# Optimization experiments

Measured on AMD Instinct MI355X. Metric: run time of the kernel, lower is better.

## Reference

```python
import jax, jax.numpy as jnp
import numpy as np

B, N, M, DN, DE, WN, WE, P = 16, 128, 1024, 512, 256, 128, 128, 512
EMB = WN + WE            # nenn embedding size per node / per edge
CLS_IN = 2 * EMB // 1    # = 2*wn + 2*we = 512
LR_OUT, CR_OUT, MR_OUT = 9, 6, 17
HID = 256


def _mk_params(key):
    ks = jax.random.split(key, 16)
    s = 0.02
    p = {
        'Wn':  jax.random.normal(ks[0], (DN, WN), jnp.float32) * s,
        'We':  jax.random.normal(ks[1], (DE, WE), jnp.float32) * s,
        'Wn2': jax.random.normal(ks[2], (DN, WN), jnp.float32) * s,
        'We2': jax.random.normal(ks[3], (DE, WE), jnp.float32) * s,
    }
    for i, h in enumerate(['scr', 'lr', 'mr']):
        out = {'scr': CR_OUT, 'lr': LR_OUT, 'mr': MR_OUT}[h]
        p[h + '_W1'] = jax.random.normal(ks[4 + 4 * i], (2 * EMB, HID), jnp.float32) * s
        p[h + '_b1'] = jnp.zeros((HID,), jnp.float32)
        p[h + '_W2'] = jax.random.normal(ks[5 + 4 * i], (HID, out), jnp.float32) * s
        p[h + '_b2'] = jnp.zeros((out,), jnp.float32)
    return p


def setup_inputs() -> dict:
    key = jax.random.key(0)
    ks = jax.random.split(key, 10)
    inp = {
        'node_features': jax.random.normal(ks[0], (B, N, DN), jnp.float32),
        'edge_features': jax.random.normal(ks[1], (B, N, N, DE), jnp.float32),
        'adj_mat': (jax.random.uniform(ks[2], (B, N, N)) < 0.1).astype(jnp.float32),
        'line_adj_mat': (jax.random.uniform(ks[3], (B, M, M)) < 0.02).astype(jnp.float32),
        'edge_index': jax.random.randint(ks[4], (B, 2, M), 0, N, jnp.int32),
        'object_pairs': jax.random.randint(ks[5], (B, P, 2), 0, N, jnp.int32),
        'num_obj': jax.random.randint(ks[6], (B,), N // 4, N + 1, jnp.int32),
        'num_edges': jax.random.randint(ks[7], (B,), M // 4, M + 1, jnp.int32),
    }
    inp.update(_mk_params(ks[8]))
    return inp


def _mlp(x, W1, b1, W2, b2):
    return jax.nn.relu(x @ W1 + b1) @ W2 + b2


def _forward(node_features, edge_features, adj_mat, line_adj_mat,
             Wn, We, Wn2, We2,
             scr_W1, scr_b1, scr_W2, scr_b2,
             lr_W1, lr_b1, lr_W2, lr_b2,
             mr_W1, mr_b1, mr_W2, mr_b2,
             edge_index, object_pairs, num_obj, num_edges):
    dt = node_features.dtype
    # ragged slicing [:num_obj] / [:num_edges] expressed as masks (padding stays 0)
    nmask = (jnp.arange(N) < num_obj[:, None]).astype(dt)      # [B,N]
    emask = (jnp.arange(M) < num_edges[:, None]).astype(dt)    # [B,M]

    X = node_features * nmask[..., None]                        # [B,N,DN]
    A = (adj_mat * nmask[:, :, None] * nmask[:, None, :]
         + jnp.eye(N, dtype=dt)[None] * nmask[:, :, None])      # A + I, masked
    h = jax.nn.relu((A @ X) @ Wn) * nmask[..., None]            # [B,N,WN] node-level emb

    src, dst = edge_index[:, 0], edge_index[:, 1]               # [B,M]
    Eg = jax.vmap(lambda e, s, d: e[s, d])(edge_features, src, dst)  # [B,M,DE]
    Eg = Eg * emask[..., None]
    L = (line_adj_mat * emask[:, :, None] * emask[:, None, :]
         + jnp.eye(M, dtype=dt)[None] * emask[:, :, None])      # line graph A + I
    g = jax.nn.relu((L @ Eg) @ We) * emask[..., None]           # [B,M,WE] edge-level emb

    # aggregate edge embeddings onto their source nodes (ragged scatter-add)
    agg = jax.vmap(lambda gb, sb: jnp.zeros((N, WE), gb.dtype).at[sb].add(gb))(g, src)
    node_emb = jnp.concatenate([h, agg * nmask[..., None]], -1)  # [B,N,EMB]

    # dense pairwise edge embeddings [B,N,N,EMB]
    Xp = X @ Wn2                                                 # [B,N,WN]
    Pm = jax.nn.relu(Xp[:, :, None, :] + Xp[:, None, :, :])      # node part [B,N,N,WN]
    Q = jax.nn.relu(edge_features @ We2)                         # edge part [B,N,N,WE]
    edge_emb = jnp.concatenate([Pm, Q], -1)

    # make_classifier_inputs: fused ragged gather instead of python double loop
    p0, p1 = object_pairs[..., 0], object_pairs[..., 1]          # [B,P]
    emb0 = jnp.take_along_axis(node_emb, p0[:, :, None], axis=1)  # [B,P,EMB]
    emb1 = jnp.take_along_axis(node_emb, p1[:, :, None], axis=1)
    eedge = jax.vmap(lambda eb, a, b: eb[a, b])(edge_emb, p0, p1)  # [B,P,EMB]
    ci = jnp.concatenate([emb0 + emb1, eedge], -1)               # aggregator='sum'

    lr = _mlp(ci, lr_W1, lr_b1, lr_W2, lr_b2)
    cr = _mlp(ci, scr_W1, scr_b1, scr_W2, scr_b2)
    mr = _mlp(ci, mr_W1, mr_b1, mr_W2, mr_b2)
    return lr, cr, mr


def reference(node_features, edge_features, adj_mat, line_adj_mat,
              edge_index, object_pairs, num_obj, num_edges,
              Wn, We, Wn2, We2,
              scr_W1, scr_b1, scr_W2, scr_b2,
              lr_W1, lr_b1, lr_W2, lr_b2,
              mr_W1, mr_b1, mr_W2, mr_b2):
    return _forward(node_features, edge_features, adj_mat, line_adj_mat,
                    Wn, We, Wn2, We2,
                    scr_W1, scr_b1, scr_W2, scr_b2,
                    lr_W1, lr_b1, lr_W2, lr_b2,
                    mr_W1, mr_b1, mr_W2, mr_b2,
                    edge_index, object_pairs, num_obj, num_edges)
```

## Files before the change

### kernel.cpp

```cpp
#include <hip/hip_runtime.h>
#include <hip/hip_bf16.h>
#include <cstdint>
#include <cstddef>

#define BB 16
#define NN 128
#define MM 1024
#define DN 512
#define DE 256
#define WN 128
#define WE 128
#define PP 512
#define HIDW 256
#define CIW 512

typedef __attribute__((ext_vector_type(8))) short s16x8;
typedef __attribute__((ext_vector_type(4))) float f32x4;

__device__ __forceinline__ float bf2f(unsigned short u) {
    unsigned int x = ((unsigned int)u) << 16;
    union { unsigned int i; float f; } c; c.i = x; return c.f;
}
__device__ __forceinline__ short f2b(float f) {
    __hip_bfloat16 h = __float2bfloat16(f);
    return *reinterpret_cast<short*>(&h);
}

__device__ __forceinline__ void gl_lds16(const ushort* g, ushort* l) {
    __builtin_amdgcn_global_load_lds(
        (const __attribute__((address_space(1))) unsigned int*)g,
        (__attribute__((address_space(3))) unsigned int*)l,
        16, 0, 0);
}

__global__ __launch_bounds__(256) void k0_prep(
    const float* __restrict__ lrW1, const float* __restrict__ scrW1,
    const float* __restrict__ mrW1,
    const float* __restrict__ lrb1, const float* __restrict__ scrb1,
    const float* __restrict__ mrb1,
    const float* __restrict__ Wn, const float* __restrict__ Wn2,
    const float* __restrict__ We, const float* __restrict__ We2,
    __hip_bfloat16* __restrict__ W1t, __hip_bfloat16* __restrict__ WncT,
    __hip_bfloat16* __restrict__ WeT, __hip_bfloat16* __restrict__ We2T,
    float* __restrict__ b1cat)
{
    int blk = blockIdx.x;
    int t = threadIdx.x;
    if (blk < 768) {
        int h = blk >> 8, n = blk & 255;
        const float* W = (h == 0) ? lrW1 : (h == 1) ? scrW1 : mrW1;
        W1t[(size_t)blk * 512 + t]       = __float2bfloat16(W[t * 256 + n]);
        W1t[(size_t)blk * 512 + t + 256] = __float2bfloat16(W[(t + 256) * 256 + n]);
    } else if (blk == 768) {
        b1cat[t]       = lrb1[t];
        b1cat[256 + t] = scrb1[t];
        b1cat[512 + t] = mrb1[t];
    } else if (blk < 897) {
        int n = blk - 769;
        WeT[(size_t)n * 256 + t] = __float2bfloat16(We[t * 128 + n]);
    } else if (blk < 1153) {
        int n = blk - 897;
        const float* W = (n < 128) ? Wn : Wn2;
        int c = n & 127;
        WncT[(size_t)n * 512 + t]       = __float2bfloat16(W[t * 128 + c]);
        WncT[(size_t)n * 512 + t + 256] = __float2bfloat16(W[(t + 256) * 128 + c]);
    } else {
        int n = blk - 1153;
        We2T[(size_t)n * 256 + t] = __float2bfloat16(We2[t * 128 + n]);
    }
}

__global__ __launch_bounds__(256) void fproj(
    const float* __restrict__ nf, const float* __restrict__ ef,
    const int* __restrict__ eidx, const int* __restrict__ opair,
    const int* __restrict__ nobj, const int* __restrict__ nedg,
    const ushort* __restrict__ WncT, const ushort* __restrict__ WeT,
    const ushort* __restrict__ We2T,
    float* __restrict__ Y, float* __restrict__ Xp,
    float* __restrict__ G1, __hip_bfloat16* __restrict__ ci)
{
    __shared__ ushort As[128 * 32];
    __shared__ ushort Bs[128 * 32];
    __shared__ unsigned rowoff[128];
    __shared__ float    rowval[128];

    int blk = blockIdx.x;
    int route, mb, nb, K;
    const ushort* Bt;
    if (blk < 32)       { route = 0; mb = blk >> 1;  nb = blk & 1; K = 512; Bt = WncT; }
    else if (blk < 160) { route = 1; mb = blk - 32;  nb = 0;       K = 256; Bt = WeT;  }
    else                { route = 2; mb = blk - 160; nb = 0;       K = 256; Bt = We2T; }
    int row0 = mb * 128, col0 = nb * 128;
    int t = threadIdx.x;

    if (t < 128) {
        int r = row0 + t;
        unsigned off; float valid = 1.f;
        if (route == 0) {
            int b = r >> 7, i = r & 127;
            off = (unsigned)r * DN;
            valid = (i < nobj[b]) ? 1.f : 0.f;
        } else if (route == 1) {
            int b = r >> 10, m = r & 1023;
            int src = eidx[b * 2 * MM + m];
            int dst = eidx[b * 2 * MM + MM + m];
            off = (unsigned)((b * NN + src) * NN + dst) * DE;
            valid = (m < nedg[b]) ? 1.f : 0.f;
        } else {
            int r2 = r;
            int b = r2 >> 9, p = r2 & 511;
            int i0 = opair[(b * PP + p) * 2];
            int i1 = opair[(b * PP + p) * 2 + 1];
            off = (unsigned)((b * NN + i0) * NN + i1) * DE;
        }
        rowoff[t] = off; rowval[t] = valid;
    }

    const float* Asrc = (route == 0) ? nf : ef;
    int lane = t & 63;
    int w    = t >> 6;
    int wr   = w >> 1, wc = w & 1;
    int arow = w * 32 + (lane >> 2);
    int ak   = (lane & 3) * 8;
    int qk   = (lane >> 4) * 8;
    int fr   = lane & 15;
    int sr   = t >> 2;
    int sk   = (t & 3) * 8;
    f32x4 acc[4][4];
    #pragma unroll
    for (int i = 0; i < 4; ++i)
        #pragma unroll
        for (int j = 0; j < 4; ++j) acc[i][j] = (f32x4){0.f, 0.f, 0.f, 0.f};

    for (int k0 = 0; k0 < K; k0 += 32) {
        __syncthreads();
        gl_lds16(&Bt[(size_t)(col0 + sr) * K + k0 + sk],      &Bs[t * 8]);
        gl_lds16(&Bt[(size_t)(col0 + sr + 64) * K + k0 + sk], &Bs[t * 8 + 2048]);
        {
            unsigned o0 = rowoff[arow] + k0 + ak;
            unsigned o1 = rowoff[arow + 16] + k0 + ak;
            float m0 = rowval[arow], m1 = rowval[arow + 16];
            float4 a0 = *(const float4*)&Asrc[o0];
            float4 a1 = *(const float4*)&Asrc[o0 + 4];
            float4 b0 = *(const float4*)&Asrc[o1];
            float4 b1 = *(const float4*)&Asrc[o1 + 4];
            s16x8 pa, pb;
            pa[0]=f2b(a0.x*m0); pa[1]=f2b(a0.y*m0); pa[2]=f2b(a0.z*m0); pa[3]=f2b(a0.w*m0);
            pa[4]=f2b(a1.x*m0); pa[5]=f2b(a1.y*m0); pa[6]=f2b(a1.z*m0); pa[7]=f2b(a1.w*m0);
            pb[0]=f2b(b0.x*m1); pb[1]=f2b(b0.y*m1); pb[2]=f2b(b0.z*m1); pb[3]=f2b(b0.w*m1);
            pb[4]=f2b(b1.x*m1); pb[5]=f2b(b1.y*m1); pb[6]=f2b(b1.z*m1); pb[7]=f2b(b1.w*m1);
            *(s16x8*)&As[arow * 32 + ak]        = pa;
            *(s16x8*)&As[(arow + 16) * 32 + ak] = pb;
        }
        __syncthreads();
        s16x8 af[4], bfv[4];
        #pragma unroll
        for (int mi = 0; mi < 4; ++mi)
            af[mi] = *(const s16x8*)&As[(wr * 64 + mi * 16 + fr) * 32 + qk];
        #pragma unroll
        for (int ni = 0; ni < 4; ++ni)
            bfv[ni] = *(const s16x8*)&Bs[(wc * 64 + ni * 16 + fr) * 32 + qk];
        #pragma unroll
        for (int mi = 0; mi < 4; ++mi)
            #pragma unroll
            for (int ni = 0; ni < 4; ++ni)
                acc[mi][ni] = __builtin_amdgcn_mfma_f32_16x16x32_bf16(
                    af[mi], bfv[ni], acc[mi][ni], 0, 0, 0);
    }
    int crow = (lane >> 4) * 4;
    #pragma unroll
    for (int mi = 0; mi < 4; ++mi) {
        #pragma unroll
        for (int ni = 0; ni < 4; ++ni) {
            int gc = col0 + wc * 64 + ni * 16 + fr;
            int gr = row0 + wr * 64 + mi * 16 + crow;
            #pragma unroll
            for (int rg = 0; rg < 4; ++rg) {
                float v = acc[mi][ni][rg];
                int r = gr + rg;
                if (route == 0) {
                    if (gc < 128) Y [(size_t)r * WN + gc]       = v;
                    else          Xp[(size_t)r * WN + gc - 128] = v;
                } else if (route == 1) {
                    G1[(size_t)r * WE + gc] = v;
                } else {
                    ci[(size_t)r * CIW + 384 + gc] = __float2bfloat16(fmaxf(v, 0.f));
                }
            }
        }
    }
}

__global__ __launch_bounds__(256) void k2_gcn_node(
    const float* __restrict__ adj, const int* __restrict__ num_obj,
    const float* __restrict__ Y, float* __restrict__ node_emb)
{
    __shared__ float As[16 * 129];
    int b  = blockIdx.x >> 4;
    int i0 = ((blockIdx.x >> 1) & 7) * 16;
    int ch = blockIdx.x & 1;
    int s  = num_obj[b];
    int t  = threadIdx.x;
    if (t < 128) {
        for (int rr = 0; rr < 16; ++rr) {
            int i = i0 + rr;
            float v = 0.f;
            if (i < s) {
                v = adj[(size_t)(b * NN + i) * NN + t] * ((t < s) ? 1.f : 0.f);
                if (t == i) v += 1.f;
            }
            As[rr * 129 + t] = v;
        }
    }
    __syncthreads();
    int c  = ch * 64 + (t & 63);
    int rb = (t >> 6) * 4;
    float acc[4] = {0.f,0.f,0.f,0.f};
    for (int j = 0; j < NN; ++j) {
        float yv = Y[(b * NN + j) * WN + c];
        #pragma unroll
        for (int r = 0; r < 4; ++r) acc[r] += As[(rb + r) * 129 + j] * yv;
    }
    #pragma unroll
    for (int r = 0; r < 4; ++r) {
        int i = i0 + rb + r;
        node_emb[(b * NN + i) * 256 + c]       = fmaxf(acc[r], 0.f);
        node_emb[(b * NN + i) * 256 + 128 + c] = 0.f;
    }
}

__global__ __launch_bounds__(128) void k4_line_gcn(
    const float* __restrict__ la, const float* __restrict__ G1,
    const int* __restrict__ eidx, const int* __restrict__ num_edges,
    float* __restrict__ node_emb)
{
    int b = blockIdx.x >> 10;
    int m = blockIdx.x & 1023;
    int se = num_edges[b];
    if (m >= se) return;
    __shared__ int   cnt;
    __shared__ int   idxs[MM];
    __shared__ float vals[MM];
    int t = threadIdx.x;
    if (t == 0) cnt = 0;
    __syncthreads();
    const float* larow = la + ((size_t)b * MM + m) * MM;
    for (int it = 0; it < 8; ++it) {
        int j = it * 128 + t;
        float v = larow[j];
        if (v != 0.f) {
            int pos = atomicAdd(&cnt, 1);
            idxs[pos] = j;
            vals[pos] = v;
        }
    }
    __syncthreads();
    int n = cnt;
    const float* g1b = G1 + (size_t)b * MM * WE;
    float acc = g1b[m * WE + t];
    for (int p = 0; p < n; ++p)
        acc += vals[p] * g1b[idxs[p] * WE + t];
    float g = fmaxf(acc, 0.f);
    int src = eidx[b * 2 * MM + m];
    atomicAdd(&node_emb[(b * NN + src) * 256 + 128 + t], g);
}

__global__ __launch_bounds__(256) void k5a_build_ci(
    const float* __restrict__ node_emb, const float* __restrict__ Xp,
    const int* __restrict__ opairs, const int* __restrict__ num_obj,
    __hip_bfloat16* __restrict__ ci)
{
    __shared__ int   pi0[16], pi1[16];
    __shared__ float nm0[16], nm1[16];
    int b     = blockIdx.x >> 5;
    int pbase = (blockIdx.x & 31) * 16;
    int t     = threadIdx.x;
    int s     = num_obj[b];
    if (t < 16) {
        int p  = pbase + t;
        int i0 = opairs[(b * PP + p) * 2];
        int i1 = opairs[(b * PP + p) * 2 + 1];
        pi0[t] = i0; pi1[t] = i1;
        nm0[t] = (i0 < s) ? 1.f : 0.f;
        nm1[t] = (i1 < s) ? 1.f : 0.f;
    }
    __syncthreads();
    for (int pp = 0; pp < 16; ++pp) {
        int i0 = pi0[pp], i1 = pi1[pp];
        int p  = pbase + pp;
        __hip_bfloat16* cirow = ci + (size_t)(b * PP + p) * CIW;
        float m0f = (t < 128) ? 1.f : nm0[pp];
        float m1f = (t < 128) ? 1.f : nm1[pp];
        float v = node_emb[(b * NN + i0) * 256 + t] * m0f
                + node_emb[(b * NN + i1) * 256 + t] * m1f;
        cirow[t] = __float2bfloat16(v);
        if (t < 128) {
            float pm = Xp[(b * NN + i0) * WN + t] + Xp[(b * NN + i1) * WN + t];
            cirow[256 + t] = __float2bfloat16(fmaxf(pm, 0.f));
        }
    }
}

__global__ __launch_bounds__(256) void k6_mlp1_mfma(
    const ushort* __restrict__ A,
    const ushort* __restrict__ Bt,
    const float* __restrict__ b1cat,
    __hip_bfloat16* __restrict__ H)
{
    __shared__ ushort As[128 * 32];
    __shared__ ushort Bs[128 * 32];
    int t    = threadIdx.x;
    int col0 = blockIdx.x * 128;
    int row0 = blockIdx.y * 128;
    int lane = t & 63;
    int w    = t >> 6;
    int wr   = w >> 1, wc = w & 1;
    int qk   = (lane >> 4) * 8;
    int fr   = lane & 15;
    int sr   = t >> 2;
    int sk   = (t & 3) * 8;
    f32x4 acc[4][4];
    #pragma unroll
    for (int i = 0; i < 4; ++i)
        #pragma unroll
        for (int j = 0; j < 4; ++j) acc[i][j] = (f32x4){0.f, 0.f, 0.f, 0.f};

    for (int k0 = 0; k0 < CIW; k0 += 32) {
        __syncthreads();
        gl_lds16(&A [(size_t)(row0 + sr) * CIW + k0 + sk],      &As[t * 8]);
        gl_lds16(&A [(size_t)(row0 + sr + 64) * CIW + k0 + sk], &As[t * 8 + 2048]);
        gl_lds16(&Bt[(size_t)(col0 + sr) * CIW + k0 + sk],      &Bs[t * 8]);
        gl_lds16(&Bt[(size_t)(col0 + sr + 64) * CIW + k0 + sk], &Bs[t * 8 + 2048]);
        __syncthreads();
        s16x8 af[4], bfv[4];
        #pragma unroll
        for (int mi = 0; mi < 4; ++mi)
            af[mi] = *(const s16x8*)&As[(wr * 64 + mi * 16 + fr) * 32 + qk];
        #pragma unroll
        for (int ni = 0; ni < 4; ++ni)
            bfv[ni] = *(const s16x8*)&Bs[(wc * 64 + ni * 16 + fr) * 32 + qk];
        #pragma unroll
        for (int mi = 0; mi < 4; ++mi)
            #pragma unroll
            for (int ni = 0; ni < 4; ++ni)
                acc[mi][ni] = __builtin_amdgcn_mfma_f32_16x16x32_bf16(
                    af[mi], bfv[ni], acc[mi][ni], 0, 0, 0);
    }
    int crow = (lane >> 4) * 4;
    #pragma unroll
    for (int mi = 0; mi < 4; ++mi) {
        #pragma unroll
        for (int ni = 0; ni < 4; ++ni) {
            int gc = col0 + wc * 64 + ni * 16 + fr;
            int gr = row0 + wr * 64 + mi * 16 + crow;
            float bias = b1cat[gc];
            #pragma unroll
            for (int rg = 0; rg < 4; ++rg) {
                float v = fmaxf(acc[mi][ni][rg] + bias, 0.f);
                H[(size_t)(gr + rg) * 768 + gc] = __float2bfloat16(v);
            }
        }
    }
}

__global__ __launch_bounds__(256) void k7_mlp2(
    const __hip_bfloat16* __restrict__ H,
    const float* __restrict__ lrW2, const float* __restrict__ lrb2,
    const float* __restrict__ scrW2, const float* __restrict__ scrb2,
    const float* __restrict__ mrW2, const float* __restrict__ mrb2,
    float* __restrict__ outp)
{
    __shared__ float w2s[32 * 257];
    int t = threadIdx.x;
    for (int o = 0; o < 32; ++o) {
        float v;
        if (o < 9)       v = lrW2[t * 9 + o];
        else if (o < 15) v = scrW2[t * 6 + (o - 9)];
        else             v = mrW2[t * 17 + (o - 15)];
        w2s[o * 257 + t] = v;
    }
    __syncthreads();
    int p = blockIdx.x * 8 + (t >> 5);
    int o = t & 31;
    int seg = (o < 9) ? 0 : ((o < 15) ? 1 : 2);
    const ushort* hr = (const ushort*)H + (size_t)p * 768 + seg * 256;
    const float* wr = &w2s[o * 257];
    float acc = (o < 9) ? lrb2[o] : ((o < 15) ? scrb2[o - 9] : mrb2[o - 15]);
    for (int k = 0; k < HIDW; k += 8) {
        s16x8 u = *(const s16x8*)&hr[k];
        acc += bf2f((unsigned short)u[0]) * wr[k]
             + bf2f((unsigned short)u[1]) * wr[k + 1]
             + bf2f((unsigned short)u[2]) * wr[k + 2]
             + bf2f((unsigned short)u[3]) * wr[k + 3]
             + bf2f((unsigned short)u[4]) * wr[k + 4]
             + bf2f((unsigned short)u[5]) * wr[k + 5]
             + bf2f((unsigned short)u[6]) * wr[k + 6]
             + bf2f((unsigned short)u[7]) * wr[k + 7];
    }
    if (o < 9)       outp[(size_t)p * 9 + o] = acc;
    else if (o < 15) outp[8192 * 9 + (size_t)p * 6 + (o - 9)] = acc;
    else             outp[8192 * 15 + (size_t)p * 17 + (o - 15)] = acc;
}

extern "C" void kernel_launch(void* const* d_in, const int* in_sizes, int n_in,
                              void* d_out, int out_size, void* d_ws, size_t ws_size,
                              hipStream_t stream) {
    const float* nf    = (const float*)d_in[0];
    const float* ef    = (const float*)d_in[1];
    const float* adj   = (const float*)d_in[2];
    const float* la    = (const float*)d_in[3];
    const int*   eidx  = (const int*)d_in[4];
    const int*   opair = (const int*)d_in[5];
    const int*   nobj  = (const int*)d_in[6];
    const int*   nedg  = (const int*)d_in[7];
    const float* Wn    = (const float*)d_in[8];
    const float* We    = (const float*)d_in[9];
    const float* Wn2   = (const float*)d_in[10];
    const float* We2   = (const float*)d_in[11];
    const float* scrW1 = (const float*)d_in[12];
    const float* scrb1 = (const float*)d_in[13];
    const float* scrW2 = (const float*)d_in[14];
    const float* scrb2 = (const float*)d_in[15];
    const float* lrW1  = (const float*)d_in[16];
    const float* lrb1  = (const float*)d_in[17];
    const float* lrW2  = (const float*)d_in[18];
    const float* lrb2  = (const float*)d_in[19];
    const float* mrW1  = (const float*)d_in[20];
    const float* mrb1  = (const float*)d_in[21];
    const float* mrW2  = (const float*)d_in[22];
    const float* mrb2  = (const float*)d_in[23];

    float* ws = (float*)d_ws;
    float* Y        = ws;
    float* Xp       = Y + 262144;
    float* node_emb = Xp + 262144;
    float* G1       = node_emb + 524288;
    float* base     = G1 + 2097152;
    __hip_bfloat16* ci   = (__hip_bfloat16*)base;
    __hip_bfloat16* hid  = (__hip_bfloat16*)(base + 2097152);
    __hip_bfloat16* W1t  = (__hip_bfloat16*)(base + 2097152 + 3145728);
    __hip_bfloat16* WncT = (__hip_bfloat16*)(base + 2097152 + 3145728 + 196608);
    __hip_bfloat16* WeT  = (__hip_bfloat16*)(base + 2097152 + 3145728 + 196608 + 65536);
    __hip_bfloat16* We2T = (__hip_bfloat16*)(base + 2097152 + 3145728 + 196608 + 65536 + 16384);
    float* b1cat = base + 2097152 + 3145728 + 196608 + 65536 + 16384 + 16384;

    k0_prep <<<1281, 256, 0, stream>>>(lrW1, scrW1, mrW1, lrb1, scrb1, mrb1,
                                       Wn, Wn2, We, We2,
                                       W1t, WncT, WeT, We2T, b1cat);
    fproj   <<<224, 256, 0, stream>>>(nf, ef, eidx, opair, nobj, nedg,
                                      (const ushort*)WncT, (const ushort*)WeT,
                                      (const ushort*)We2T, Y, Xp, G1, ci);
    k2_gcn_node <<<BB * 8 * 2, 256, 0, stream>>>(adj, nobj, Y, node_emb);
    k4_line_gcn <<<BB * MM, 128, 0, stream>>>(la, G1, eidx, nedg, node_emb);
    k5a_build_ci<<<BB * (PP / 16), 256, 0, stream>>>(node_emb, Xp, opair, nobj, ci);
    k6_mlp1_mfma<<<dim3(6, 64), 256, 0, stream>>>((const ushort*)ci,
                                                  (const ushort*)W1t, b1cat, hid);
    k7_mlp2     <<<8192 / 8, 256, 0, stream>>>(hid, lrW2, lrb2, scrW2, scrb2,
                                               mrW2, mrb2, (float*)d_out);
}
```

Baseline: 473.1 us.

## Fuse all stages into one persistent kernel with software grid barriers

Replaces the seven separate kernel launches with a single persistent kernel of 384 blocks. Each former kernel becomes a phase that loops over its virtual blocks, and phases are separated by an atomic-counter grid barrier that is reset by a memset before launch. This is meant to remove launch overhead and the gaps between dependent kernels. In exchange, each phase is limited to 384 resident blocks, the kernel needs more LDS because it uses a union of all phase buffers, and correctness relies on every block being co-resident; the spin loop has a bounded timeout that silently breaks out.

```diff
diff --git a/kernel.cpp b/kernel.cpp
--- a/kernel.cpp
+++ b/kernel.cpp
@@ -14,6 +14,8 @@
 #define HIDW 256
 #define CIW 512
 
+#define NBLK 384
+
 typedef __attribute__((ext_vector_type(8))) short s16x8;
 typedef __attribute__((ext_vector_type(4))) float f32x4;
 
@@ -25,7 +27,6 @@
     __hip_bfloat16 h = __float2bfloat16(f);
     return *reinterpret_cast<short*>(&h);
 }
-
 __device__ __forceinline__ void gl_lds16(const ushort* g, ushort* l) {
     __builtin_amdgcn_global_load_lds(
         (const __attribute__((address_space(1))) unsigned int*)g,
@@ -33,403 +34,383 @@
         16, 0, 0);
 }
 
-__global__ __launch_bounds__(256) void k0_prep(
-    const float* __restrict__ lrW1, const float* __restrict__ scrW1,
-    const float* __restrict__ mrW1,
-    const float* __restrict__ lrb1, const float* __restrict__ scrb1,
-    const float* __restrict__ mrb1,
-    const float* __restrict__ Wn, const float* __restrict__ Wn2,
-    const float* __restrict__ We, const float* __restrict__ We2,
-    __hip_bfloat16* __restrict__ W1t, __hip_bfloat16* __restrict__ WncT,
-    __hip_bfloat16* __restrict__ WeT, __hip_bfloat16* __restrict__ We2T,
-    float* __restrict__ b1cat)
-{
-    int blk = blockIdx.x;
-    int t = threadIdx.x;
-    if (blk < 768) {
-        int h = blk >> 8, n = blk & 255;
-        const float* W = (h == 0) ? lrW1 : (h == 1) ? scrW1 : mrW1;
-        W1t[(size_t)blk * 512 + t]       = __float2bfloat16(W[t * 256 + n]);
-        W1t[(size_t)blk * 512 + t + 256] = __float2bfloat16(W[(t + 256) * 256 + n]);
-    } else if (blk == 768) {
-        b1cat[t]       = lrb1[t];
-        b1cat[256 + t] = scrb1[t];
-        b1cat[512 + t] = mrb1[t];
-    } else if (blk < 897) {
-        int n = blk - 769;
-        WeT[(size_t)n * 256 + t] = __float2bfloat16(We[t * 128 + n]);
-    } else if (blk < 1153) {
-        int n = blk - 897;
-        const float* W = (n < 128) ? Wn : Wn2;
-        int c = n & 127;
-        WncT[(size_t)n * 512 + t]       = __float2bfloat16(W[t * 128 + c]);
-        WncT[(size_t)n * 512 + t + 256] = __float2bfloat16(W[(t + 256) * 128 + c]);
-    } else {
-        int n = blk - 1153;
-        We2T[(size_t)n * 256 + t] = __float2bfloat16(We2[t * 128 + n]);
-    }
-}
-
-__global__ __launch_bounds__(256) void fproj(
-    const float* __restrict__ nf, const float* __restrict__ ef,
-    const int* __restrict__ eidx, const int* __restrict__ opair,
-    const int* __restrict__ nobj, const int* __restrict__ nedg,
-    const ushort* __restrict__ WncT, const ushort* __restrict__ WeT,
-    const ushort* __restrict__ We2T,
-    float* __restrict__ Y, float* __restrict__ Xp,
-    float* __restrict__ G1, __hip_bfloat16* __restrict__ ci)
-{
-    __shared__ ushort As[128 * 32];
-    __shared__ ushort Bs[128 * 32];
-    __shared__ unsigned rowoff[128];
-    __shared__ float    rowval[128];
-
-    int blk = blockIdx.x;
-    int route, mb, nb, K;
-    const ushort* Bt;
-    if (blk < 32)       { route = 0; mb = blk >> 1;  nb = blk & 1; K = 512; Bt = WncT; }
-    else if (blk < 160) { route = 1; mb = blk - 32;  nb = 0;       K = 256; Bt = WeT;  }
-    else                { route = 2; mb = blk - 160; nb = 0;       K = 256; Bt = We2T; }
-    int row0 = mb * 128, col0 = nb * 128;
-    int t = threadIdx.x;
-
-    if (t < 128) {
-        int r = row0 + t;
-        unsigned off; float valid = 1.f;
-        if (route == 0) {
-            int b = r >> 7, i = r & 127;
-            off = (unsigned)r * DN;
-            valid = (i < nobj[b]) ? 1.f : 0.f;
-        } else if (route == 1) {
-            int b = r >> 10, m = r & 1023;
-            int src = eidx[b * 2 * MM + m];
-            int dst = eidx[b * 2 * MM + MM + m];
-            off = (unsigned)((b * NN + src) * NN + dst) * DE;
-            valid = (m < nedg[b]) ? 1.f : 0.f;
+__device__ __forceinline__ void grid_barrier(unsigned* cnt, unsigned phase) {
+    __syncthreads();
+    if (threadIdx.x == 0) {
+        __threadfence();
+        __hip_atomic_fetch_add(cnt, 1u, __ATOMIC_ACQ_REL, __HIP_MEMORY_SCOPE_AGENT);
+        unsigned target = (unsigned)NBLK * (phase + 1u);
+        long spin = 0;
+        while (__hip_atomic_load(cnt, __ATOMIC_ACQUIRE, __HIP_MEMORY_SCOPE_AGENT) < target) {
+            __builtin_amdgcn_s_sleep(8);
+            if (++spin > (1L << 20)) break;
+        }
+        __threadfence();
+    }
+    __syncthreads();
+}
+
+struct MegaP {
+    const float *nf, *ef, *adj, *la;
+    const int *eidx, *opair, *nobj, *nedg;
+    const float *Wn, *We, *Wn2, *We2;
+    const float *scrW1, *scrb1, *scrW2, *scrb2;
+    const float *lrW1, *lrb1, *lrW2, *lrb2;
+    const float *mrW1, *mrb1, *mrW2, *mrb2;
+    float *Y, *Xp, *node_emb, *G1;
+    __hip_bfloat16 *ci, *hid, *W1t, *WncT, *WeT, *We2T;
+    float *b1cat;
+    unsigned *gbar;
+    float *outp;
+};
+
+union Smem {
+    struct { ushort As[128 * 32]; ushort Bs[128 * 32];
+             unsigned rowoff[128]; float rowval[128]; } g;
+    struct { float As[16 * 129]; } k2;
+    struct { int idxs[2][MM]; float vals[2][MM]; int cnt[2]; } k4;
+    struct { int pi0[16], pi1[16]; float nm0[16], nm1[16]; } k5;
+    struct { float w2s[32 * 257]; } k7;
+};
+
+__global__ __launch_bounds__(256, 2) void mega(MegaP P) {
+    __shared__ Smem S;
+    const int t   = threadIdx.x;
+    const int bid = blockIdx.x;
+    const int nb  = gridDim.x;
+
+    for (int vb = bid; vb < 1281; vb += nb) {
+        if (vb < 768) {
+            int h = vb >> 8, n = vb & 255;
+            const float* W = (h == 0) ? P.lrW1 : (h == 1) ? P.scrW1 : P.mrW1;
+            P.W1t[(size_t)vb * 512 + t]       = __float2bfloat16(W[t * 256 + n]);
+            P.W1t[(size_t)vb * 512 + t + 256] = __float2bfloat16(W[(t + 256) * 256 + n]);
+        } else if (vb == 768) {
+            P.b1cat[t]       = P.lrb1[t];
+            P.b1cat[256 + t] = P.scrb1[t];
+            P.b1cat[512 + t] = P.mrb1[t];
+        } else if (vb < 897) {
+            int n = vb - 769;
+            P.WeT[(size_t)n * 256 + t] = __float2bfloat16(P.We[t * 128 + n]);
+        } else if (vb < 1153) {
+            int n = vb - 897;
+            const float* W = (n < 128) ? P.Wn : P.Wn2;
+            int c = n & 127;
+            P.WncT[(size_t)n * 512 + t]       = __float2bfloat16(W[t * 128 + c]);
+            P.WncT[(size_t)n * 512 + t + 256] = __float2bfloat16(W[(t + 256) * 128 + c]);
         } else {
-            int r2 = r;
-            int b = r2 >> 9, p = r2 & 511;
-            int i0 = opair[(b * PP + p) * 2];
-            int i1 = opair[(b * PP + p) * 2 + 1];
-            off = (unsigned)((b * NN + i0) * NN + i1) * DE;
-        }
-        rowoff[t] = off; rowval[t] = valid;
-    }
-
-    const float* Asrc = (route == 0) ? nf : ef;
-    int lane = t & 63;
-    int w    = t >> 6;
-    int wr   = w >> 1, wc = w & 1;
-    int arow = w * 32 + (lane >> 2);
-    int ak   = (lane & 3) * 8;
-    int qk   = (lane >> 4) * 8;
-    int fr   = lane & 15;
-    int sr   = t >> 2;
-    int sk   = (t & 3) * 8;
-    f32x4 acc[4][4];
-    #pragma unroll
-    for (int i = 0; i < 4; ++i)
+            int n = vb - 1153;
+            P.We2T[(size_t)n * 256 + t] = __float2bfloat16(P.We2[t * 128 + n]);
+        }
+    }
+    grid_barrier(P.gbar, 0);
+
+    {
+        const int lane = t & 63, w = t >> 6;
+        const int wr = w >> 1, wc = w & 1;
+        const int arow = w * 32 + (lane >> 2);
+        const int ak = (lane & 3) * 8;
+        const int qk = (lane >> 4) * 8;
+        const int fr = lane & 15;
+        const int sr = t >> 2;
+        const int sk = (t & 3) * 8;
+        for (int vb = bid; vb < 224; vb += nb) {
+            int route, mb, nbk, K;
+            const ushort* Bt;
+            if (vb < 32)       { route = 0; mb = vb >> 1;  nbk = vb & 1; K = 512; Bt = (const ushort*)P.WncT; }
+            else if (vb < 160) { route = 1; mb = vb - 32;  nbk = 0;      K = 256; Bt = (const ushort*)P.WeT;  }
+            else               { route = 2; mb = vb - 160; nbk = 0;      K = 256; Bt = (const ushort*)P.We2T; }
+            int row0 = mb * 128, col0 = nbk * 128;
+            __syncthreads();
+            if (t < 128) {
+                int r = row0 + t;
+                unsigned off; float valid = 1.f;
+                if (route == 0) {
+                    int b = r >> 7, i = r & 127;
+                    off = (unsigned)r * DN;
+                    valid = (i < P.nobj[b]) ? 1.f : 0.f;
+                } else if (route == 1) {
+                    int b = r >> 10, m = r & 1023;
+                    int src = P.eidx[b * 2 * MM + m];
+                    int dst = P.eidx[b * 2 * MM + MM + m];
+                    off = (unsigned)((b * NN + src) * NN + dst) * DE;
+                    valid = (m < P.nedg[b]) ? 1.f : 0.f;
+                } else {
+                    int b = r >> 9, p = r & 511;
+                    int i0 = P.opair[(b * PP + p) * 2];
+                    int i1 = P.opair[(b * PP + p) * 2 + 1];
+                    off = (unsigned)((b * NN + i0) * NN + i1) * DE;
+                }
+                S.g.rowoff[t] = off; S.g.rowval[t] = valid;
+            }
+            const float* Asrc = (route == 0) ? P.nf : P.ef;
+            f32x4 acc[4][4];
+            #pragma unroll
+            for (int i = 0; i < 4; ++i)
+                #pragma unroll
+                for (int j = 0; j < 4; ++j) acc[i][j] = (f32x4){0.f, 0.f, 0.f, 0.f};
+
+            for (int k0 = 0; k0 < K; k0 += 32) {
+                __syncthreads();
+                gl_lds16(&Bt[(size_t)(col0 + sr) * K + k0 + sk],      &S.g.Bs[t * 8]);
+                gl_lds16(&Bt[(size_t)(col0 + sr + 64) * K + k0 + sk], &S.g.Bs[t * 8 + 2048]);
+                {
+                    unsigned o0 = S.g.rowoff[arow] + k0 + ak;
+                    unsigned o1 = S.g.rowoff[arow + 16] + k0 + ak;
+                    float m0 = S.g.rowval[arow], m1 = S.g.rowval[arow + 16];
+                    float4 a0 = *(const float4*)&Asrc[o0];
+                    float4 a1 = *(const float4*)&Asrc[o0 + 4];
+                    float4 b0 = *(const float4*)&Asrc[o1];
+                    float4 b1 = *(const float4*)&Asrc[o1 + 4];
+                    s16x8 pa, pb;
+                    pa[0]=f2b(a0.x*m0); pa[1]=f2b(a0.y*m0); pa[2]=f2b(a0.z*m0); pa[3]=f2b(a0.w*m0);
+                    pa[4]=f2b(a1.x*m0); pa[5]=f2b(a1.y*m0); pa[6]=f2b(a1.z*m0); pa[7]=f2b(a1.w*m0);
+                    pb[0]=f2b(b0.x*m1); pb[1]=f2b(b0.y*m1); pb[2]=f2b(b0.z*m1); pb[3]=f2b(b0.w*m1);
+                    pb[4]=f2b(b1.x*m1); pb[5]=f2b(b1.y*m1); pb[6]=f2b(b1.z*m1); pb[7]=f2b(b1.w*m1);
+                    *(s16x8*)&S.g.As[arow * 32 + ak]        = pa;
+                    *(s16x8*)&S.g.As[(arow + 16) * 32 + ak] = pb;
+                }
+                __syncthreads();
+                s16x8 af[4], bfv[4];
+                #pragma unroll
+                for (int mi = 0; mi < 4; ++mi)
+                    af[mi] = *(const s16x8*)&S.g.As[(wr * 64 + mi * 16 + fr) * 32 + qk];
+                #pragma unroll
+                for (int ni = 0; ni < 4; ++ni)
+                    bfv[ni] = *(const s16x8*)&S.g.Bs[(wc * 64 + ni * 16 + fr) * 32 + qk];
+                #pragma unroll
+                for (int mi = 0; mi < 4; ++mi)
+                    #pragma unroll
+                    for (int ni = 0; ni < 4; ++ni)
+                        acc[mi][ni] = __builtin_amdgcn_mfma_f32_16x16x32_bf16(
+                            af[mi], bfv[ni], acc[mi][ni], 0, 0, 0);
+            }
+            int crow = (lane >> 4) * 4;
+            #pragma unroll
+            for (int mi = 0; mi < 4; ++mi) {
+                #pragma unroll
+                for (int ni = 0; ni < 4; ++ni) {
+                    int gc = col0 + wc * 64 + ni * 16 + fr;
+                    int gr = row0 + wr * 64 + mi * 16 + crow;
+                    #pragma unroll
+                    for (int rg = 0; rg < 4; ++rg) {
+                        float v = acc[mi][ni][rg];
+                        int r = gr + rg;
+                        if (route == 0) {
+                            if (gc < 128) P.Y [(size_t)r * WN + gc]       = v;
+                            else          P.Xp[(size_t)r * WN + gc - 128] = v;
+                        } else if (route == 1) {
+                            P.G1[(size_t)r * WE + gc] = v;
+                        } else {
+                            P.ci[(size_t)r * CIW + 384 + gc] = __float2bfloat16(fmaxf(v, 0.f));
+                        }
+                    }
+                }
+            }
+        }
+    }
+    grid_barrier(P.gbar, 1);
+
+    for (int vb = bid; vb < 256; vb += nb) {
+        int b  = vb >> 4;
+        int i0 = ((vb >> 1) & 7) * 16;
+        int ch = vb & 1;
+        int s  = P.nobj[b];
+        __syncthreads();
+        if (t < 128) {
+            for (int rr = 0; rr < 16; ++rr) {
+                int i = i0 + rr;
+                float v = 0.f;
+                if (i < s) {
+                    v = P.adj[(size_t)(b * NN + i) * NN + t] * ((t < s) ? 1.f : 0.f);
+                    if (t == i) v += 1.f;
+                }
+                S.k2.As[rr * 129 + t] = v;
+            }
+        }
+        __syncthreads();
+        int c  = ch * 64 + (t & 63);
+        int rb = (t >> 6) * 4;
+        float acc[4] = {0.f, 0.f, 0.f, 0.f};
+        for (int j = 0; j < NN; ++j) {
+            float yv = P.Y[(b * NN + j) * WN + c];
+            #pragma unroll
+            for (int r = 0; r < 4; ++r) acc[r] += S.k2.As[(rb + r) * 129 + j] * yv;
+        }
         #pragma unroll
-        for (int j = 0; j < 4; ++j) acc[i][j] = (f32x4){0.f, 0.f, 0.f, 0.f};
-
-    for (int k0 = 0; k0 < K; k0 += 32) {
+        for (int r = 0; r < 4; ++r) {
+            int i = i0 + rb + r;
+            P.node_emb[(b * NN + i) * 256 + c]       = fmaxf(acc[r], 0.f);
+            P.node_emb[(b * NN + i) * 256 + 128 + c] = 0.f;
+        }
+    }
+    grid_barrier(P.gbar, 2);
+
+    {
+        const int half = t >> 7;
+        const int ch   = t & 127;
+        for (int vb = bid; vb < 8192; vb += nb) {
+            int b = vb >> 9;
+            int m = (vb & 511) * 2 + half;
+            int se = P.nedg[b];
+            bool act = (m < se);
+            __syncthreads();
+            if (ch == 0) S.k4.cnt[half] = 0;
+            __syncthreads();
+            if (act) {
+                const float4* larow = (const float4*)(P.la + ((size_t)b * MM + m) * MM);
+                #pragma unroll
+                for (int pass = 0; pass < 2; ++pass) {
+                    int j4 = pass * 128 + ch;
+                    float4 v = larow[j4];
+                    int j0 = j4 * 4;
+                    if (v.x != 0.f) { int p = atomicAdd(&S.k4.cnt[half], 1); S.k4.idxs[half][p] = j0;     S.k4.vals[half][p] = v.x; }
+                    if (v.y != 0.f) { int p = atomicAdd(&S.k4.cnt[half], 1); S.k4.idxs[half][p] = j0 + 1; S.k4.vals[half][p] = v.y; }
+                    if (v.z != 0.f) { int p = atomicAdd(&S.k4.cnt[half], 1); S.k4.idxs[half][p] = j0 + 2; S.k4.vals[half][p] = v.z; }
+                    if (v.w != 0.f) { int p = atomicAdd(&S.k4.cnt[half], 1); S.k4.idxs[half][p] = j0 + 3; S.k4.vals[half][p] = v.w; }
+                }
+            }
+            __syncthreads();
+            if (act) {
+                int n = S.k4.cnt[half];
+                const float* g1b = P.G1 + (size_t)b * MM * WE;
+                float acc = g1b[m * WE + ch];
+                for (int p = 0; p < n; ++p)
+                    acc += S.k4.vals[half][p] * g1b[S.k4.idxs[half][p] * WE + ch];
+                float gv = fmaxf(acc, 0.f);
+                int src = P.eidx[b * 2 * MM + m];
+                atomicAdd(&P.node_emb[((size_t)b * NN + src) * 256 + 128 + ch], gv);
+            }
+        }
+    }
+    grid_barrier(P.gbar, 3);
+
+    for (int vb = bid; vb < 512; vb += nb) {
+        int b     = vb >> 5;
+        int pbase = (vb & 31) * 16;
+        int s     = P.nobj[b];
         __syncthreads();
-        gl_lds16(&Bt[(size_t)(col0 + sr) * K + k0 + sk],      &Bs[t * 8]);
-        gl_lds16(&Bt[(size_t)(col0 + sr + 64) * K + k0 + sk], &Bs[t * 8 + 2048]);
-        {
-            unsigned o0 = rowoff[arow] + k0 + ak;
-            unsigned o1 = rowoff[arow + 16] + k0 + ak;
-            float m0 = rowval[arow], m1 = rowval[arow + 16];
-            float4 a0 = *(const float4*)&Asrc[o0];
-            float4 a1 = *(const float4*)&Asrc[o0 + 4];
-            float4 b0 = *(const float4*)&Asrc[o1];
-            float4 b1 = *(const float4*)&Asrc[o1 + 4];
-            s16x8 pa, pb;
-            pa[0]=f2b(a0.x*m0); pa[1]=f2b(a0.y*m0); pa[2]=f2b(a0.z*m0); pa[3]=f2b(a0.w*m0);
-            pa[4]=f2b(a1.x*m0); pa[5]=f2b(a1.y*m0); pa[6]=f2b(a1.z*m0); pa[7]=f2b(a1.w*m0);
-            pb[0]=f2b(b0.x*m1); pb[1]=f2b(b0.y*m1); pb[2]=f2b(b0.z*m1); pb[3]=f2b(b0.w*m1);
-            pb[4]=f2b(b1.x*m1); pb[5]=f2b(b1.y*m1); pb[6]=f2b(b1.z*m1); pb[7]=f2b(b1.w*m1);
-            *(s16x8*)&As[arow * 32 + ak]        = pa;
-            *(s16x8*)&As[(arow + 16) * 32 + ak] = pb;
+        if (t < 16) {
+            int p  = pbase + t;
+            int i0 = P.opair[(b * PP + p) * 2];
+            int i1 = P.opair[(b * PP + p) * 2 + 1];
+            S.k5.pi0[t] = i0; S.k5.pi1[t] = i1;
+            S.k5.nm0[t] = (i0 < s) ? 1.f : 0.f;
+            S.k5.nm1[t] = (i1 < s) ? 1.f : 0.f;
         }
         __syncthreads();
-        s16x8 af[4], bfv[4];
-        #pragma unroll
-        for (int mi = 0; mi < 4; ++mi)
-            af[mi] = *(const s16x8*)&As[(wr * 64 + mi * 16 + fr) * 32 + qk];
-        #pragma unroll
-        for (int ni = 0; ni < 4; ++ni)
-            bfv[ni] = *(const s16x8*)&Bs[(wc * 64 + ni * 16 + fr) * 32 + qk];
-        #pragma unroll
-        for (int mi = 0; mi < 4; ++mi)
+        for (int pp = 0; pp < 16; ++pp) {
+            int i0 = S.k5.pi0[pp], i1 = S.k5.pi1[pp];
+            int p  = pbase + pp;
+            __hip_bfloat16* cirow = P.ci + (size_t)(b * PP + p) * CIW;
+            float m0f = (t < 128) ? 1.f : S.k5.nm0[pp];
+            float m1f = (t < 128) ? 1.f : S.k5.nm1[pp];
+            float v = P.node_emb[(b * NN + i0) * 256 + t] * m0f
+                    + P.node_emb[(b * NN + i1) * 256 + t] * m1f;
+            cirow[t] = __float2bfloat16(v);
+            if (t < 128) {
+                float pm = P.Xp[(b * NN + i0) * WN + t] + P.Xp[(b * NN + i1) * WN + t];
+                cirow[256 + t] = __float2bfloat16(fmaxf(pm, 0.f));
+            }
+        }
+    }
+    grid_barrier(P.gbar, 4);
+
+    {
+        const int lane = t & 63, w = t >> 6;
+        const int wr = w >> 1, wc = w & 1;
+        const int qk = (lane >> 4) * 8;
+        const int fr = lane & 15;
+        const int sr = t >> 2;
+        const int sk = (t & 3) * 8;
+        const ushort* A  = (const ushort*)P.ci;
+        const ushort* Bt = (const ushort*)P.W1t;
+        for (int vb = bid; vb < 384; vb += nb) {
+            int col0 = (vb % 6) * 128;
+            int row0 = (vb / 6) * 128;
+            f32x4 acc[4][4];
             #pragma unroll
-            for (int ni = 0; ni < 4; ++ni)
-                acc[mi][ni] = __builtin_amdgcn_mfma_f32_16x16x32_bf16(
-                    af[mi], bfv[ni], acc[mi][ni], 0, 0, 0);
-    }
-    int crow = (lane >> 4) * 4;
-    #pragma unroll
-    for (int mi = 0; mi < 4; ++mi) {
-        #pragma unroll
-        for (int ni = 0; ni < 4; ++ni) {
-            int gc = col0 + wc * 64 + ni * 16 + fr;
-            int gr = row0 + wr * 64 + mi * 16 + crow;
+            for (int i = 0; i < 4; ++i)
+                #pragma unroll
+                for (int j = 0; j < 4; ++j) acc[i][j] = (f32x4){0.f, 0.f, 0.f, 0.f};
+            for (int k0 = 0; k0 < CIW; k0 += 32) {
+                __syncthreads();
+                gl_lds16(&A [(size_t)(row0 + sr) * CIW + k0 + sk],      &S.g.As[t * 8]);
+                gl_lds16(&A [(size_t)(row0 + sr + 64) * CIW + k0 + sk], &S.g.As[t * 8 + 2048]);
+                gl_lds16(&Bt[(size_t)(col0 + sr) * CIW + k0 + sk],      &S.g.Bs[t * 8]);
+                gl_lds16(&Bt[(size_t)(col0 + sr + 64) * CIW + k0 + sk], &S.g.Bs[t * 8 + 2048]);
+                __syncthreads();
+                s16x8 af[4], bfv[4];
+                #pragma unroll
+                for (int mi = 0; mi < 4; ++mi)
+                    af[mi] = *(const s16x8*)&S.g.As[(wr * 64 + mi * 16 + fr) * 32 + qk];
+                #pragma unroll
+                for (int ni = 0; ni < 4; ++ni)
+                    bfv[ni] = *(const s16x8*)&S.g.Bs[(wc * 64 + ni * 16 + fr) * 32 + qk];
+                #pragma unroll
+                for (int mi = 0; mi < 4; ++mi)
+                    #pragma unroll
+                    for (int ni = 0; ni < 4; ++ni)
+                        acc[mi][ni] = __builtin_amdgcn_mfma_f32_16x16x32_bf16(
+                            af[mi], bfv[ni], acc[mi][ni], 0, 0, 0);
+            }
+            int crow = (lane >> 4) * 4;
             #pragma unroll
-            for (int rg = 0; rg < 4; ++rg) {
-                float v = acc[mi][ni][rg];
-                int r = gr + rg;
-                if (route == 0) {
-                    if (gc < 128) Y [(size_t)r * WN + gc]       = v;
-                    else          Xp[(size_t)r * WN + gc - 128] = v;
-                } else if (route == 1) {
-                    G1[(size_t)r * WE + gc] = v;
-                } else {
-                    ci[(size_t)r * CIW + 384 + gc] = __float2bfloat16(fmaxf(v, 0.f));
-                }
-            }
-        }
-    }
-}
-
-__global__ __launch_bounds__(256) void k2_gcn_node(
-    const float* __restrict__ adj, const int* __restrict__ num_obj,
-    const float* __restrict__ Y, float* __restrict__ node_emb)
-{
-    __shared__ float As[16 * 129];
-    int b  = blockIdx.x >> 4;
-    int i0 = ((blockIdx.x >> 1) & 7) * 16;
-    int ch = blockIdx.x & 1;
-    int s  = num_obj[b];
-    int t  = threadIdx.x;
-    if (t < 128) {
-        for (int rr = 0; rr < 16; ++rr) {
-            int i = i0 + rr;
-            float v = 0.f;
-            if (i < s) {
-                v = adj[(size_t)(b * NN + i) * NN + t] * ((t < s) ? 1.f : 0.f);
-                if (t == i) v += 1.f;
-            }
-            As[rr * 129 + t] = v;
-        }
-    }
-    __syncthreads();
-    int c  = ch * 64 + (t & 63);
-    int rb = (t >> 6) * 4;
-    float acc[4] = {0.f,0.f,0.f,0.f};
-    for (int j = 0; j < NN; ++j) {
-        float yv = Y[(b * NN + j) * WN + c];
-        #pragma unroll
-        for (int r = 0; r < 4; ++r) acc[r] += As[(rb + r) * 129 + j] * yv;
-    }
-    #pragma unroll
-    for (int r = 0; r < 4; ++r) {
-        int i = i0 + rb + r;
-        node_emb[(b * NN + i) * 256 + c]       = fmaxf(acc[r], 0.f);
-        node_emb[(b * NN + i) * 256 + 128 + c] = 0.f;
-    }
-}
-
-__global__ __launch_bounds__(128) void k4_line_gcn(
-    const float* __restrict__ la, const float* __restrict__ G1,
-    const int* __restrict__ eidx, const int* __restrict__ num_edges,
-    float* __restrict__ node_emb)
-{
-    int b = blockIdx.x >> 10;
-    int m = blockIdx.x & 1023;
-    int se = num_edges[b];
-    if (m >= se) return;
-    __shared__ int   cnt;
-    __shared__ int   idxs[MM];
-    __shared__ float vals[MM];
-    int t = threadIdx.x;
-    if (t == 0) cnt = 0;
-    __syncthreads();
-    const float* larow = la + ((size_t)b * MM + m) * MM;
-    for (int it = 0; it < 8; ++it) {
-        int j = it * 128 + t;
-        float v = larow[j];
-        if (v != 0.f) {
-            int pos = atomicAdd(&cnt, 1);
-            idxs[pos] = j;
-            vals[pos] = v;
-        }
-    }
-    __syncthreads();
-    int n = cnt;
-    const float* g1b = G1 + (size_t)b * MM * WE;
-    float acc = g1b[m * WE + t];
-    for (int p = 0; p < n; ++p)
-        acc += vals[p] * g1b[idxs[p] * WE + t];
-    float g = fmaxf(acc, 0.f);
-    int src = eidx[b * 2 * MM + m];
-    atomicAdd(&node_emb[(b * NN + src) * 256 + 128 + t], g);
-}
-
-__global__ __launch_bounds__(256) void k5a_build_ci(
-    const float* __restrict__ node_emb, const float* __restrict__ Xp,
-    const int* __restrict__ opairs, const int* __restrict__ num_obj,
-    __hip_bfloat16* __restrict__ ci)
-{
-    __shared__ int   pi0[16], pi1[16];
-    __shared__ float nm0[16], nm1[16];
-    int b     = blockIdx.x >> 5;
-    int pbase = (blockIdx.x & 31) * 16;
-    int t     = threadIdx.x;
-    int s     = num_obj[b];
-    if (t < 16) {
-        int p  = pbase + t;
-        int i0 = opairs[(b * PP + p) * 2];
-        int i1 = opairs[(b * PP + p) * 2 + 1];
-        pi0[t] = i0; pi1[t] = i1;
-        nm0[t] = (i0 < s) ? 1.f : 0.f;
-        nm1[t] = (i1 < s) ? 1.f : 0.f;
-    }
-    __syncthreads();
-    for (int pp = 0; pp < 16; ++pp) {
-        int i0 = pi0[pp], i1 = pi1[pp];
-        int p  = pbase + pp;
-        __hip_bfloat16* cirow = ci + (size_t)(b * PP + p) * CIW;
-        float m0f = (t < 128) ? 1.f : nm0[pp];
-        float m1f = (t < 128) ? 1.f : nm1[pp];
-        float v = node_emb[(b * NN + i0) * 256 + t] * m0f
-                + node_emb[(b * NN + i1) * 256 + t] * m1f;
-        cirow[t] = __float2bfloat16(v);
-        if (t < 128) {
-            float pm = Xp[(b * NN + i0) * WN + t] + Xp[(b * NN + i1) * WN + t];
-            cirow[256 + t] = __float2bfloat16(fmaxf(pm, 0.f));
-        }
-    }
-}
-
-__global__ __launch_bounds__(256) void k6_mlp1_mfma(
-    const ushort* __restrict__ A,
-    const ushort* __restrict__ Bt,
-    const float* __restrict__ b1cat,
-    __hip_bfloat16* __restrict__ H)
-{
-    __shared__ ushort As[128 * 32];
-    __shared__ ushort Bs[128 * 32];
-    int t    = threadIdx.x;
-    int col0 = blockIdx.x * 128;
-    int row0 = blockIdx.y * 128;
-    int lane = t & 63;
-    int w    = t >> 6;
-    int wr   = w >> 1, wc = w & 1;
-    int qk   = (lane >> 4) * 8;
-    int fr   = lane & 15;
-    int sr   = t >> 2;
-    int sk   = (t & 3) * 8;
-    f32x4 acc[4][4];
-    #pragma unroll
-    for (int i = 0; i < 4; ++i)
-        #pragma unroll
-        for (int j = 0; j < 4; ++j) acc[i][j] = (f32x4){0.f, 0.f, 0.f, 0.f};
-
-    for (int k0 = 0; k0 < CIW; k0 += 32) {
+            for (int mi = 0; mi < 4; ++mi) {
+                #pragma unroll
+                for (int ni = 0; ni < 4; ++ni) {
+                    int gc = col0 + wc * 64 + ni * 16 + fr;
+                    int gr = row0 + wr * 64 + mi * 16 + crow;
+                    float bias = P.b1cat[gc];
+                    #pragma unroll
+                    for (int rg = 0; rg < 4; ++rg) {
+                        float v = fmaxf(acc[mi][ni][rg] + bias, 0.f);
+                        P.hid[(size_t)(gr + rg) * 768 + gc] = __float2bfloat16(v);
+                    }
+                }
+            }
+        }
+    }
+    grid_barrier(P.gbar, 5);
+
+    {
+        for (int o = 0; o < 32; ++o) {
+            float v;
+            if (o < 9)       v = P.lrW2[t * 9 + o];
+            else if (o < 15) v = P.scrW2[t * 6 + (o - 9)];
+            else             v = P.mrW2[t * 17 + (o - 15)];
+            S.k7.w2s[o * 257 + t] = v;
+        }
         __syncthreads();
-        gl_lds16(&A [(size_t)(row0 + sr) * CIW + k0 + sk],      &As[t * 8]);
-        gl_lds16(&A [(size_t)(row0 + sr + 64) * CIW + k0 + sk], &As[t * 8 + 2048]);
-        gl_lds16(&Bt[(size_t)(col0 + sr) * CIW + k0 + sk],      &Bs[t * 8]);
-        gl_lds16(&Bt[(size_t)(col0 + sr + 64) * CIW + k0 + sk], &Bs[t * 8 + 2048]);
-        __syncthreads();
-        s16x8 af[4], bfv[4];
-        #pragma unroll
-        for (int mi = 0; mi < 4; ++mi)
-            af[mi] = *(const s16x8*)&As[(wr * 64 + mi * 16 + fr) * 32 + qk];
-        #pragma unroll
-        for (int ni = 0; ni < 4; ++ni)
-            bfv[ni] = *(const s16x8*)&Bs[(wc * 64 + ni * 16 + fr) * 32 + qk];
-        #pragma unroll
-        for (int mi = 0; mi < 4; ++mi)
-            #pragma unroll
-            for (int ni = 0; ni < 4; ++ni)
-                acc[mi][ni] = __builtin_amdgcn_mfma_f32_16x16x32_bf16(
-                    af[mi], bfv[ni], acc[mi][ni], 0, 0, 0);
-    }
-    int crow = (lane >> 4) * 4;
-    #pragma unroll
-    for (int mi = 0; mi < 4; ++mi) {
-        #pragma unroll
-        for (int ni = 0; ni < 4; ++ni) {
-            int gc = col0 + wc * 64 + ni * 16 + fr;
-            int gr = row0 + wr * 64 + mi * 16 + crow;
-            float bias = b1cat[gc];
-            #pragma unroll
-            for (int rg = 0; rg < 4; ++rg) {
-                float v = fmaxf(acc[mi][ni][rg] + bias, 0.f);
-                H[(size_t)(gr + rg) * 768 + gc] = __float2bfloat16(v);
-            }
-        }
-    }
-}
-
-__global__ __launch_bounds__(256) void k7_mlp2(
-    const __hip_bfloat16* __restrict__ H,
-    const float* __restrict__ lrW2, const float* __restrict__ lrb2,
-    const float* __restrict__ scrW2, const float* __restrict__ scrb2,
-    const float* __restrict__ mrW2, const float* __restrict__ mrb2,
-    float* __restrict__ outp)
-{
-    __shared__ float w2s[32 * 257];
-    int t = threadIdx.x;
-    for (int o = 0; o < 32; ++o) {
-        float v;
-        if (o < 9)       v = lrW2[t * 9 + o];
-        else if (o < 15) v = scrW2[t * 6 + (o - 9)];
-        else             v = mrW2[t * 17 + (o - 15)];
-        w2s[o * 257 + t] = v;
-    }
-    __syncthreads();
-    int p = blockIdx.x * 8 + (t >> 5);
-    int o = t & 31;
-    int seg = (o < 9) ? 0 : ((o < 15) ? 1 : 2);
-    const ushort* hr = (const ushort*)H + (size_t)p * 768 + seg * 256;
-    const float* wr = &w2s[o * 257];
-    float acc = (o < 9) ? lrb2[o] : ((o < 15) ? scrb2[o - 9] : mrb2[o - 15]);
-    for (int k = 0; k < HIDW; k += 8) {
-        s16x8 u = *(const s16x8*)&hr[k];
-        acc += bf2f((unsigned short)u[0]) * wr[k]
-             + bf2f((unsigned short)u[1]) * wr[k + 1]
-             + bf2f((unsigned short)u[2]) * wr[k + 2]
-             + bf2f((unsigned short)u[3]) * wr[k + 3]
-             + bf2f((unsigned short)u[4]) * wr[k + 4]
-             + bf2f((unsigned short)u[5]) * wr[k + 5]
-             + bf2f((unsigned short)u[6]) * wr[k + 6]
-             + bf2f((unsigned short)u[7]) * wr[k + 7];
-    }
-    if (o < 9)       outp[(size_t)p * 9 + o] = acc;
-    else if (o < 15) outp[8192 * 9 + (size_t)p * 6 + (o - 9)] = acc;
-    else             outp[8192 * 15 + (size_t)p * 17 + (o - 15)] = acc;
+        int o = t & 31;
+        int seg = (o < 9) ? 0 : ((o < 15) ? 1 : 2);
+        const float* wr = &S.k7.w2s[o * 257];
+        float bias = (o < 9) ? P.lrb2[o] : ((o < 15) ? P.scrb2[o - 9] : P.mrb2[o - 15]);
+        for (int vb = bid; vb < 1024; vb += nb) {
+            int p = vb * 8 + (t >> 5);
+            const ushort* hr = (const ushort*)P.hid + (size_t)p * 768 + seg * 256;
+            float acc = bias;
+            for (int k = 0; k < HIDW; k += 8) {
+                s16x8 u = *(const s16x8*)&hr[k];
+                acc += bf2f((unsigned short)u[0]) * wr[k]
+                     + bf2f((unsigned short)u[1]) * wr[k + 1]
+                     + bf2f((unsigned short)u[2]) * wr[k + 2]
+                     + bf2f((unsigned short)u[3]) * wr[k + 3]
+                     + bf2f((unsigned short)u[4]) * wr[k + 4]
+                     + bf2f((unsigned short)u[5]) * wr[k + 5]
+                     + bf2f((unsigned short)u[6]) * wr[k + 6]
+                     + bf2f((unsigned short)u[7]) * wr[k + 7];
+            }
+            if (o < 9)       P.outp[(size_t)p * 9 + o] = acc;
+            else if (o < 15) P.outp[8192 * 9 + (size_t)p * 6 + (o - 9)] = acc;
+            else             P.outp[8192 * 15 + (size_t)p * 17 + (o - 15)] = acc;
+        }
+    }
 }
 
 extern "C" void kernel_launch(void* const* d_in, const int* in_sizes, int n_in,
                               void* d_out, int out_size, void* d_ws, size_t ws_size,
                               hipStream_t stream) {
-    const float* nf    = (const float*)d_in[0];
-    const float* ef    = (const float*)d_in[1];
-    const float* adj   = (const float*)d_in[2];
-    const float* la    = (const float*)d_in[3];
-    const int*   eidx  = (const int*)d_in[4];
-    const int*   opair = (const int*)d_in[5];
-    const int*   nobj  = (const int*)d_in[6];
-    const int*   nedg  = (const int*)d_in[7];
-    const float* Wn    = (const float*)d_in[8];
-    const float* We    = (const float*)d_in[9];
-    const float* Wn2   = (const float*)d_in[10];
-    const float* We2   = (const float*)d_in[11];
-    const float* scrW1 = (const float*)d_in[12];
-    const float* scrb1 = (const float*)d_in[13];
-    const float* scrW2 = (const float*)d_in[14];
-    const float* scrb2 = (const float*)d_in[15];
-    const float* lrW1  = (const float*)d_in[16];
-    const float* lrb1  = (const float*)d_in[17];
-    const float* lrW2  = (const float*)d_in[18];
-    const float* lrb2  = (const float*)d_in[19];
-    const float* mrW1  = (const float*)d_in[20];
-    const float* mrb1  = (const float*)d_in[21];
-    const float* mrW2  = (const float*)d_in[22];
-    const float* mrb2  = (const float*)d_in[23];
-
     float* ws = (float*)d_ws;
     float* Y        = ws;
     float* Xp       = Y + 262144;
@@ -443,18 +424,39 @@
     __hip_bfloat16* WeT  = (__hip_bfloat16*)(base + 2097152 + 3145728 + 196608 + 65536);
     __hip_bfloat16* We2T = (__hip_bfloat16*)(base + 2097152 + 3145728 + 196608 + 65536 + 16384);
     float* b1cat = base + 2097152 + 3145728 + 196608 + 65536 + 16384 + 16384;
-
-    k0_prep <<<1281, 256, 0, stream>>>(lrW1, scrW1, mrW1, lrb1, scrb1, mrb1,
-                                       Wn, Wn2, We, We2,
-                                       W1t, WncT, WeT, We2T, b1cat);
-    fproj   <<<224, 256, 0, stream>>>(nf, ef, eidx, opair, nobj, nedg,
-                                      (const ushort*)WncT, (const ushort*)WeT,
-                                      (const ushort*)We2T, Y, Xp, G1, ci);
-    k2_gcn_node <<<BB * 8 * 2, 256, 0, stream>>>(adj, nobj, Y, node_emb);
-    k4_line_gcn <<<BB * MM, 128, 0, stream>>>(la, G1, eidx, nedg, node_emb);
-    k5a_build_ci<<<BB * (PP / 16), 256, 0, stream>>>(node_emb, Xp, opair, nobj, ci);
-    k6_mlp1_mfma<<<dim3(6, 64), 256, 0, stream>>>((const ushort*)ci,
-                                                  (const ushort*)W1t, b1cat, hid);
-    k7_mlp2     <<<8192 / 8, 256, 0, stream>>>(hid, lrW2, lrb2, scrW2, scrb2,
-                                               mrW2, mrb2, (float*)d_out);
-}
+    unsigned* gbar = (unsigned*)(b1cat + 1024);
+
+    MegaP hp;
+    hp.nf    = (const float*)d_in[0];
+    hp.ef    = (const float*)d_in[1];
+    hp.adj   = (const float*)d_in[2];
+    hp.la    = (const float*)d_in[3];
+    hp.eidx  = (const int*)d_in[4];
+    hp.opair = (const int*)d_in[5];
+    hp.nobj  = (const int*)d_in[6];
+    hp.nedg  = (const int*)d_in[7];
+    hp.Wn    = (const float*)d_in[8];
+    hp.We    = (const float*)d_in[9];
+    hp.Wn2   = (const float*)d_in[10];
+    hp.We2   = (const float*)d_in[11];
+    hp.scrW1 = (const float*)d_in[12];
+    hp.scrb1 = (const float*)d_in[13];
+    hp.scrW2 = (const float*)d_in[14];
+    hp.scrb2 = (const float*)d_in[15];
+    hp.lrW1  = (const float*)d_in[16];
+    hp.lrb1  = (const float*)d_in[17];
+    hp.lrW2  = (const float*)d_in[18];
+    hp.lrb2  = (const float*)d_in[19];
+    hp.mrW1  = (const float*)d_in[20];
+    hp.mrb1  = (const float*)d_in[21];
+    hp.mrW2  = (const float*)d_in[22];
+    hp.mrb2  = (const float*)d_in[23];
+    hp.Y = Y; hp.Xp = Xp; hp.node_emb = node_emb; hp.G1 = G1;
+    hp.ci = ci; hp.hid = hid; hp.W1t = W1t; hp.WncT = WncT;
+    hp.WeT = WeT; hp.We2T = We2T; hp.b1cat = b1cat;
+    hp.gbar = gbar;
+    hp.outp = (float*)d_out;
+
+    hipMemsetAsync(gbar, 0, 64, stream);
+    mega<<<dim3(NBLK), dim3(256), 0, stream>>>(hp);
+}
```

After: 1.091 ms. +130.6%, slower.
